# Performance work log

Hardware: AMD Instinct MI355X
Metric: run time of the kernel (lower is better)

The kernel has to match this reference:

```python
import jax, jax.numpy as jnp
import numpy as np

EPS = 1e-5  # BatchNorm1d default eps


def gcn_conv(x, src, dst, w, b, n):
    # src/dst already include self-loops. Symmetric normalization D^-1/2 (A+I) D^-1/2.
    deg = jnp.zeros((n,), x.dtype).at[dst].add(1.0)
    dinv = jnp.where(deg > 0, jax.lax.rsqrt(jnp.maximum(deg, 1.0)), 0.0)
    norm = dinv[src] * dinv[dst]                      # [E+N]
    h = x @ w                                          # [B, N, H]
    msg = h[:, src, :] * norm[None, :, None]           # gather + scale  [B, E+N, H]
    agg = jnp.zeros_like(h).at[:, dst, :].add(msg)     # scatter-add
    return agg + b


def batch_norm(h, gamma, beta):
    # training-mode BN over the flattened (B*N) axis, biased variance (torch BN forward)
    mu = h.mean(axis=(0, 1))
    var = ((h - mu) ** 2).mean(axis=(0, 1))
    return (h - mu) * jax.lax.rsqrt(var + EPS) * gamma + beta


def reference(x, edge_index, W1, b1, W2, b2, gamma1, beta1, gamma2, beta2, Wc, bc):
    n = x.shape[1]
    loops = jnp.arange(n)
    src = jnp.concatenate([edge_index[0], loops])
    dst = jnp.concatenate([edge_index[1], loops])
    h = jax.nn.relu(gcn_conv(x, src, dst, W1, b1, n))
    h = batch_norm(h, gamma1, beta1)
    # dropout(p=0.2) treated as identity (eval / deterministic reference)
    h = jax.nn.relu(gcn_conv(h, src, dst, W2, b2, n))
    h = batch_norm(h, gamma2, beta2)
    out = (h @ Wc + bc).squeeze(-1)                    # [B, N]
    return out


def setup_inputs() -> dict:
    key = jax.random.key(0)
    ks = jax.random.split(key, 8)
    B, N, E, F, H = 4, 20000, 320000, 64, 128
    s = lambda fan: 1.0 / np.sqrt(fan)
    return {
        "x": jax.random.normal(ks[0], (B, N, F), dtype=jnp.float32),
        "edge_index": jax.random.randint(ks[1], (2, E), 0, N, dtype=jnp.int64),
        "W1": jax.random.normal(ks[2], (F, H), dtype=jnp.float32) * s(F),
        "b1": jnp.zeros((H,), jnp.float32),
        "W2": jax.random.normal(ks[3], (H, H), dtype=jnp.float32) * s(H),
        "b2": jnp.zeros((H,), jnp.float32),
        "gamma1": jnp.ones((H,), jnp.float32),
        "beta1": jnp.zeros((H,), jnp.float32),
        "gamma2": jnp.ones((H,), jnp.float32),
        "beta2": jnp.zeros((H,), jnp.float32),
        "Wc": jax.random.normal(ks[4], (H, 1), dtype=jnp.float32) * s(H),
        "bc": jnp.zeros((1,), jnp.float32),
    }
```

## Files before the change

kernel.cpp:

```cpp
#include <hip/hip_runtime.h>

constexpr int Bb = 4;
constexpr int Nn = 20000;
constexpr int Ff = 64;
constexpr int Hh = 128;
constexpr float BN_EPS = 1e-5f;
constexpr int NSLOTS = 64;
constexpr int NB = (Nn + 1023) / 1024;

typedef __attribute__((ext_vector_type(8))) short bf16x8;
typedef __attribute__((ext_vector_type(4))) float f32x4;

__device__ inline unsigned f2bf(float f) {
    unsigned u = __float_as_uint(f);
    return (u + 0x7fffu + ((u >> 16) & 1u)) >> 16;
}
__device__ inline unsigned pack2(float lo, float hi) { return f2bf(lo) | (f2bf(hi) << 16); }
__device__ inline float bf_lo(unsigned w) { return __uint_as_float(w << 16); }
__device__ inline float bf_hi(unsigned w) { return __uint_as_float(w & 0xffff0000u); }

template <int NU>
__device__ inline void ldrow(unsigned* u, const unsigned* p) {
    if constexpr (NU == 2) { const uint2 t = *(const uint2*)p; u[0] = t.x; u[1] = t.y; }
    else { const uint4 t = *(const uint4*)p; u[0] = t.x; u[1] = t.y; u[2] = t.z; u[3] = t.w; }
}
template <int NU>
__device__ inline void acc_row(float* a, const unsigned* u, float nm) {
#pragma unroll
    for (int c = 0; c < NU; ++c) {
        a[2 * c]     = fmaf(nm, bf_lo(u[c]), a[2 * c]);
        a[2 * c + 1] = fmaf(nm, bf_hi(u[c]), a[2 * c + 1]);
    }
}

__global__ __launch_bounds__(256) void k_pre(const int* __restrict__ dst, int E,
                                             int NDEG,
                                             int* __restrict__ deg,
                                             const float* __restrict__ x,
                                             unsigned* __restrict__ xb,
                                             const float* __restrict__ W1,
                                             unsigned short* __restrict__ WTf) {
    const int b = blockIdx.x;
    if (b < NDEG) {
        const int e = b * 256 + threadIdx.x;
        if (e < E) atomicAdd(&deg[dst[e]], 1);
    } else if (b < NDEG + (Bb * Nn * 32) / 256) {
        const int o = (b - NDEG) * 256 + threadIdx.x;
        const int n   = o >> 7;
        const int rem = o & 127;
        const int bb  = rem >> 5;
        const int c2  = rem & 31;
        const float2 v = *(const float2*)&x[(((size_t)bb * Nn + n) * 64) + c2 * 2];
        xb[o] = pack2(v.x, v.y);
    } else {
        const int f = (b - NDEG - (Bb * Nn * 32) / 256) * 256 + threadIdx.x;
        if (f < 128 * Ff) {
            const int j = f & 7, lane = (f >> 3) & 63, rest = f >> 9;
            const int ks = rest & 1, tt = rest >> 1;
            const int col = tt * 16 + (lane & 15);
            const int k = ks * 32 + ((lane >> 4) << 3) + j;
            WTf[f] = (unsigned short)f2bf(W1[(size_t)k * 128 + col]);
        }
    }
}

__global__ __launch_bounds__(1024) void k_scanall(const int* __restrict__ deg,
                                                  int* __restrict__ rowptr,
                                                  int* __restrict__ cursor,
                                                  float* __restrict__ dinv) {
    __shared__ int red[16];
    __shared__ int woff[16];
    __shared__ int base_s;
    const int tid = threadIdx.x, lane = tid & 63, wid = tid >> 6;
    const int b = blockIdx.x;

    int pre = 0;
    for (int i = tid; i < b * 1024; i += 1024) pre += deg[i] + 1;
#pragma unroll
    for (int d = 32; d; d >>= 1) pre += __shfl_down(pre, d);
    if (lane == 0) red[wid] = pre;
    __syncthreads();
    if (tid == 0) {
        int s = 0;
        for (int w = 0; w < 16; ++w) s += red[w];
        base_s = s;
    }

    const int i = b * 1024 + tid;
    const int cnt = (i < Nn) ? deg[i] + 1 : 0;
    int v = cnt;
#pragma unroll
    for (int d = 1; d < 64; d <<= 1) {
        const int t = __shfl_up(v, d);
        if (lane >= d) v += t;
    }
    __syncthreads();
    if (lane == 63) red[wid] = v;
    __syncthreads();
    if (wid == 0) {
        const int orig = (lane < 16) ? red[lane] : 0;
        int w = orig;
#pragma unroll
        for (int d = 1; d < 16; d <<= 1) {
            const int t = __shfl_up(w, d);
            if (lane >= d) w += t;
        }
        if (lane < 16) woff[lane] = w - orig;
    }
    __syncthreads();
    if (i < Nn) {
        const int excl = base_s + woff[wid] + (v - cnt);
        rowptr[i] = excl;
        cursor[i] = excl;
        dinv[i] = rsqrtf((float)cnt);
        if (i == Nn - 1) rowptr[Nn] = excl + cnt;
    }
}

__global__ void k_fill(const int* __restrict__ src, const int* __restrict__ dst, int E,
                       const float* __restrict__ dinv, int* __restrict__ cursor,
                       int* __restrict__ csr_src, float* __restrict__ csr_norm,
                       float* __restrict__ nsum) {
    int t = blockIdx.x * blockDim.x + threadIdx.x;
    int s, d;
    if (t < E) { s = src[t]; d = dst[t]; }
    else if (t < E + Nn) { s = d = t - E; }
    else return;
    int pos = atomicAdd(&cursor[d], 1);
    const float nm = dinv[s] * dinv[d];
    csr_src[pos]  = s;
    csr_norm[pos] = nm;
    atomicAdd(&nsum[d], nm);
}

__global__ __launch_bounds__(256) void k_stat(const unsigned* __restrict__ h,
                                              float* __restrict__ gsum,
                                              float* __restrict__ gsq) {
    __shared__ float lsum[128], lsq[128];
    const int tid = threadIdx.x;
    if (tid < 128) { lsum[tid] = 0.f; lsq[tid] = 0.f; }
    __syncthreads();
    constexpr int TOTAL = Bb * Nn * (Hh / 2);
    const int stride = gridDim.x * 256;
    float s0 = 0.f, s1 = 0.f, q0 = 0.f, q1 = 0.f;
    for (int i = blockIdx.x * 256 + tid; i < TOTAL; i += stride) {
        const unsigned w = h[i];
        const float lo = bf_lo(w), hi = bf_hi(w);
        s0 += lo; s1 += hi;
        q0 = fmaf(lo, lo, q0); q1 = fmaf(hi, hi, q1);
    }
    const int c0 = (tid & 63) * 2;
    atomicAdd(&lsum[c0], s0);     atomicAdd(&lsum[c0 + 1], s1);
    atomicAdd(&lsq[c0],  q0);     atomicAdd(&lsq[c0 + 1],  q1);
    __syncthreads();
    float* gs = gsum + (size_t)(blockIdx.x & (NSLOTS - 1)) * 128;
    float* gq = gsq  + (size_t)(blockIdx.x & (NSLOTS - 1)) * 128;
    if (tid < 128) { atomicAdd(&gs[tid], lsum[tid]); atomicAdd(&gq[tid], lsq[tid]); }
}

__global__ __launch_bounds__(128) void k_prep2(const float* __restrict__ gsum,
                                               const float* __restrict__ gsq,
                                               const float* __restrict__ gamma,
                                               const float* __restrict__ beta,
                                               const float* __restrict__ W2,
                                               unsigned short* __restrict__ WT2f,
                                               float* __restrict__ shW2) {
    __shared__ float sc_s[128], sh_s[128];
    const int c = threadIdx.x;
    float s = 0.f, q = 0.f;
    for (int j = 0; j < NSLOTS; ++j) { s += gsum[j * 128 + c]; q += gsq[j * 128 + c]; }
    const float inv = 1.0f / (float)(Bb * Nn);
    const float mu  = s * inv;
    const float var = q * inv - mu * mu;
    const float sc  = gamma[c] * rsqrtf(var + BN_EPS);
    sc_s[c] = sc;
    sh_s[c] = beta[c] - mu * sc;
    __syncthreads();
    if (blockIdx.x < 64) {
#pragma unroll
        for (int i = 0; i < 2; ++i) {
            const int f = blockIdx.x * 256 + i * 128 + c;
            const int j = f & 7, lane = (f >> 3) & 63, rest = f >> 9;
            const int ks = rest & 3, tt = rest >> 2;
            const int col = tt * 16 + (lane & 15);
            const int k = ks * 32 + ((lane >> 4) << 3) + j;
            WT2f[f] = (unsigned short)f2bf(sc_s[k] * W2[(size_t)k * 128 + col]);
        }
    } else {
        float a = 0.f;
        for (int k = 0; k < 128; ++k) a = fmaf(sh_s[k], W2[(size_t)k * 128 + c], a);
        shW2[c] = a;
    }
}

template <int K, bool L2E>
__global__ __launch_bounds__(128, 8) void k_fmm(const unsigned* __restrict__ G,
                                                const int* __restrict__ rowptr,
                                                const int* __restrict__ csr_src,
                                                const float* __restrict__ csr_norm,
                                                const unsigned short* __restrict__ WTf,
                                                const float* __restrict__ bias,
                                                const float* __restrict__ nsum,
                                                const float* __restrict__ shW2,
                                                unsigned short* __restrict__ Yout) {
    constexpr int NKS = K / 32;
    constexpr int AST = K + 8;
    constexpr int NU = K / 32;
    constexpr int UNR = (K == 128) ? 4 : 8;
    constexpr int ROWU = Bb * K / 2;
    constexpr int WSLOT = 16 * AST + (K == 64 ? 1024 : 0);
    __shared__ alignas(16) unsigned short sAall[2 * WSLOT];

    const int w = threadIdx.x >> 6;
    const int lane = threadIdx.x & 63;
    unsigned short* const sA = &sAall[w * WSLOT];
    unsigned short* const sO = (K == 64) ? &sA[16 * AST] : &sA[8 * AST];

    const int cg = lane & 15, kg = lane >> 4;
    const int g = blockIdx.x * 2 + w;
    const int row0 = g * 8;

#pragma unroll
    for (int j = 0; j < 2; ++j) {
        const int v = g * 2 + j;
        const int beg = rowptr[v], end = rowptr[v + 1];
        float a[2 * NU];
#pragma unroll
        for (int c = 0; c < 2 * NU; ++c) a[c] = 0.f;
        int e = beg;
        for (; e + UNR <= end; e += UNR) {
            unsigned u[UNR][NU];
            int si[UNR];
#pragma unroll
            for (int q = 0; q < UNR; ++q) si[q] = csr_src[e + q];
#pragma unroll
            for (int q = 0; q < UNR; ++q)
                ldrow<NU>(u[q], G + (size_t)si[q] * ROWU + lane * NU);
#pragma unroll
            for (int q = 0; q < UNR; ++q) acc_row<NU>(a, u[q], csr_norm[e + q]);
        }
        for (; e < end; ++e) {
            unsigned u[NU];
            ldrow<NU>(u, G + (size_t)csr_src[e] * ROWU + lane * NU);
            acc_row<NU>(a, u, csr_norm[e]);
        }
        const int row = j * 4 + kg;
        unsigned p[NU];
#pragma unroll
        for (int c = 0; c < NU; ++c) p[c] = pack2(a[2 * c], a[2 * c + 1]);
        if constexpr (NU == 2) *(uint2*)&sA[row * AST + cg * 4] = *(const uint2*)p;
        else                   *(uint4*)&sA[row * AST + cg * 8] = *(const uint4*)p;
    }

    f32x4 acc[8];
#pragma unroll
    for (int t = 0; t < 8; ++t) acc[t] = (f32x4){0.f, 0.f, 0.f, 0.f};
#pragma unroll
    for (int ks = 0; ks < NKS; ++ks) {
        const bf16x8 av = *(const bf16x8*)&sA[cg * AST + ks * 32 + kg * 8];
#pragma unroll
        for (int t = 0; t < 8; ++t) {
            const bf16x8 bv = *(const bf16x8*)&WTf[(size_t)((t * NKS + ks) * 64 + lane) * 8];
            acc[t] = __builtin_amdgcn_mfma_f32_16x16x32_bf16(av, bv, acc[t], 0, 0, 0);
        }
    }

    if (kg < 2) {
        const int rbase = kg * 4;
        float ns = 0.f;
        if (L2E) ns = nsum[g * 2 + kg];
#pragma unroll
        for (int t = 0; t < 8; ++t) {
            const int col = t * 16 + cg;
            float badd = bias[col];
            if (L2E) badd = fmaf(ns, shW2[col], badd);
#pragma unroll
            for (int jj = 0; jj < 4; ++jj) {
                const float y = fmaxf(acc[t][jj] + badd, 0.f);
                sO[(rbase + jj) * 128 + col] = (unsigned short)f2bf(y);
            }
        }
    }
    const size_t obase = (size_t)row0 * 128;
#pragma unroll
    for (int h = 0; h < 2; ++h) {
        const int i16 = h * 64 + lane;
        *(uint4*)&Yout[obase + (size_t)i16 * 8] = *(const uint4*)&sO[i16 * 8];
    }
}

__global__ void k_bnfin2(const float* __restrict__ gsum, const float* __restrict__ gsq,
                         const float* __restrict__ gamma, const float* __restrict__ beta,
                         const float* __restrict__ Wc, const float* __restrict__ bc,
                         float* __restrict__ wcs, float* __restrict__ kc) {
    __shared__ float red[128];
    const int c = threadIdx.x;
    float s = 0.f, q = 0.f;
    for (int j = 0; j < NSLOTS; ++j) { s += gsum[j * 128 + c]; q += gsq[j * 128 + c]; }
    const float inv = 1.0f / (float)(Bb * Nn);
    const float mu  = s * inv;
    const float var = q * inv - mu * mu;
    const float sc  = gamma[c] * rsqrtf(var + BN_EPS);
    const float sh  = beta[c] - mu * sc;
    const float w   = Wc[c];
    wcs[c] = sc * w;
    red[c] = sh * w;
    __syncthreads();
    for (int st = 64; st; st >>= 1) {
        if (c < st) red[c] += red[c + st];
        __syncthreads();
    }
    if (c == 0) kc[0] = red[0] + bc[0];
}

__global__ __launch_bounds__(256) void k_cls(const unsigned* __restrict__ h2,
                                             const float* __restrict__ wcs,
                                             const float* __restrict__ kc,
                                             float* __restrict__ out) {
    __shared__ float sres[64];
    const int w = threadIdx.x >> 6;
    const int lane = threadIdx.x & 63;
    const int n0 = blockIdx.x * 16;
    const float2 wc = *(const float2*)&wcs[lane * 2];
#pragma unroll
    for (int jj = 0; jj < 4; ++jj) {
        const int node = n0 + w * 4 + jj;
#pragma unroll
        for (int b = 0; b < 4; ++b) {
            const size_t row = (size_t)node * 4 + b;
            const unsigned hv = h2[row * 64 + lane];
            float p = bf_lo(hv) * wc.x + bf_hi(hv) * wc.y;
#pragma unroll
            for (int off = 32; off; off >>= 1) p += __shfl_down(p, off);
            if (lane == 0) sres[b * 16 + w * 4 + jj] = p;
        }
    }
    __syncthreads();
    if (threadIdx.x < 64) {
        const int b = threadIdx.x >> 4, i = threadIdx.x & 15;
        out[(size_t)b * Nn + n0 + i] = sres[b * 16 + i] + kc[0];
    }
}

extern "C" void kernel_launch(void* const* d_in, const int* in_sizes, int n_in,
                              void* d_out, int out_size, void* d_ws, size_t ws_size,
                              hipStream_t stream) {
    const float* x      = (const float*)d_in[0];
    const int*   ei     = (const int*)d_in[1];
    const float* W1     = (const float*)d_in[2];
    const float* b1     = (const float*)d_in[3];
    const float* W2     = (const float*)d_in[4];
    const float* b2     = (const float*)d_in[5];
    const float* gamma1 = (const float*)d_in[6];
    const float* beta1  = (const float*)d_in[7];
    const float* gamma2 = (const float*)d_in[8];
    const float* beta2  = (const float*)d_in[9];
    const float* Wc     = (const float*)d_in[10];
    const float* bc     = (const float*)d_in[11];
    float* out = (float*)d_out;

    const int E = in_sizes[1] / 2;
    const int* src = ei;
    const int* dst = ei + E;

    char* ws = (char*)d_ws;
    size_t off = 0;
    auto alloc = [&](size_t bytes) -> char* {
        char* p = ws + off;
        off += (bytes + 255) & ~(size_t)255;
        return p;
    };
    int*      deg      = (int*)     alloc((size_t)Nn * 4);
    float*    nsum     = (float*)   alloc((size_t)Nn * 4);
    float*    gstat    = (float*)   alloc((size_t)4 * NSLOTS * 128 * 4);
    const size_t zspan = (size_t)((char*)(gstat + 4 * NSLOTS * 128) - (char*)deg);
    float* gsum1 = gstat;
    float* gsq1  = gstat + NSLOTS * 128;
    float* gsum2 = gstat + 2 * NSLOTS * 128;
    float* gsq2  = gstat + 3 * NSLOTS * 128;

    int*      cursor   = (int*)     alloc((size_t)Nn * 4);
    int*      rowptr   = (int*)     alloc((size_t)(Nn + 1) * 4);
    float*    dinv     = (float*)   alloc((size_t)Nn * 4);
    int*      csr_src  = (int*)     alloc((size_t)(E + Nn) * 4);
    float*    csr_norm = (float*)   alloc((size_t)(E + Nn) * 4);
    float*    wcs      = (float*)   alloc(128 * 4);
    float*    kc       = (float*)   alloc(256);
    unsigned short* WT1f = (unsigned short*)alloc((size_t)128 * Ff * 2);
    unsigned short* WT2f = (unsigned short*)alloc((size_t)128 * Hh * 2);
    float*          shW2 = (float*)         alloc((size_t)128 * 4);
    unsigned*       xb   = (unsigned*)      alloc((size_t)Nn * Bb * 32 * 4);
    unsigned short* h1b  = (unsigned short*)alloc((size_t)Bb * Nn * Hh * 2);
    unsigned short* h2b  = (unsigned short*)alloc((size_t)Bb * Nn * Hh * 2);

    (void)hipMemsetAsync(deg, 0, zspan, stream);

    const int NDEG = (E + 255) / 256;
    const int NCVT = (Bb * Nn * 32) / 256;
    k_pre<<<NDEG + NCVT + 32, 256, 0, stream>>>(dst, E, NDEG, deg, x, xb, W1, WT1f);
    k_scanall<<<NB, 1024, 0, stream>>>(deg, rowptr, cursor, dinv);
    k_fill<<<(E + Nn + 255) / 256, 256, 0, stream>>>(src, dst, E, dinv, cursor,
                                                     csr_src, csr_norm, nsum);

    k_fmm<Ff, false><<<Nn / 4, 128, 0, stream>>>(
        xb, rowptr, csr_src, csr_norm, WT1f, b1, nullptr, nullptr, h1b);
    k_stat<<<640, 256, 0, stream>>>((const unsigned*)h1b, gsum1, gsq1);
    k_prep2<<<65, 128, 0, stream>>>(gsum1, gsq1, gamma1, beta1, W2, WT2f, shW2);
    k_fmm<Hh, true><<<Nn / 4, 128, 0, stream>>>(
        (const unsigned*)h1b, rowptr, csr_src, csr_norm, WT2f, b2, nsum, shW2, h2b);
    k_stat<<<640, 256, 0, stream>>>((const unsigned*)h2b, gsum2, gsq2);
    k_bnfin2<<<1, Hh, 0, stream>>>(gsum2, gsq2, gamma2, beta2, Wc, bc, wcs, kc);

    k_cls<<<Nn / 16, 256, 0, stream>>>((const unsigned*)h2b, wcs, kc, out);
}
```

Measured before the change: 218.4 us.

## Fuse BatchNorm statistics into GCN aggregation-matmul epilogue, one wave per block

```diff
diff --git a/kernel.cpp b/kernel.cpp
--- a/kernel.cpp
+++ b/kernel.cpp
@@ -133,31 +133,6 @@
     atomicAdd(&nsum[d], nm);
 }
 
-__global__ __launch_bounds__(256) void k_stat(const unsigned* __restrict__ h,
-                                              float* __restrict__ gsum,
-                                              float* __restrict__ gsq) {
-    __shared__ float lsum[128], lsq[128];
-    const int tid = threadIdx.x;
-    if (tid < 128) { lsum[tid] = 0.f; lsq[tid] = 0.f; }
-    __syncthreads();
-    constexpr int TOTAL = Bb * Nn * (Hh / 2);
-    const int stride = gridDim.x * 256;
-    float s0 = 0.f, s1 = 0.f, q0 = 0.f, q1 = 0.f;
-    for (int i = blockIdx.x * 256 + tid; i < TOTAL; i += stride) {
-        const unsigned w = h[i];
-        const float lo = bf_lo(w), hi = bf_hi(w);
-        s0 += lo; s1 += hi;
-        q0 = fmaf(lo, lo, q0); q1 = fmaf(hi, hi, q1);
-    }
-    const int c0 = (tid & 63) * 2;
-    atomicAdd(&lsum[c0], s0);     atomicAdd(&lsum[c0 + 1], s1);
-    atomicAdd(&lsq[c0],  q0);     atomicAdd(&lsq[c0 + 1],  q1);
-    __syncthreads();
-    float* gs = gsum + (size_t)(blockIdx.x & (NSLOTS - 1)) * 128;
-    float* gq = gsq  + (size_t)(blockIdx.x & (NSLOTS - 1)) * 128;
-    if (tid < 128) { atomicAdd(&gs[tid], lsum[tid]); atomicAdd(&gq[tid], lsq[tid]); }
-}
-
 __global__ __launch_bounds__(128) void k_prep2(const float* __restrict__ gsum,
                                                const float* __restrict__ gsq,
                                                const float* __restrict__ gamma,
@@ -194,50 +169,57 @@
 }
 
 template <int K, bool L2E>
-__global__ __launch_bounds__(128, 8) void k_fmm(const unsigned* __restrict__ G,
-                                                const int* __restrict__ rowptr,
-                                                const int* __restrict__ csr_src,
-                                                const float* __restrict__ csr_norm,
-                                                const unsigned short* __restrict__ WTf,
-                                                const float* __restrict__ bias,
-                                                const float* __restrict__ nsum,
-                                                const float* __restrict__ shW2,
-                                                unsigned short* __restrict__ Yout) {
+__global__ __launch_bounds__(64, 6) void k_fmm(const unsigned* __restrict__ G,
+                                               const int* __restrict__ rowptr,
+                                               const int* __restrict__ csr_src,
+                                               const float* __restrict__ csr_norm,
+                                               const unsigned short* __restrict__ WTf,
+                                               const float* __restrict__ bias,
+                                               const float* __restrict__ nsum,
+                                               const float* __restrict__ shW2,
+                                               unsigned short* __restrict__ Yout,
+                                               float* __restrict__ gsum,
+                                               float* __restrict__ gsq) {
     constexpr int NKS = K / 32;
     constexpr int AST = K + 8;
     constexpr int NU = K / 32;
-    constexpr int UNR = (K == 128) ? 4 : 8;
     constexpr int ROWU = Bb * K / 2;
-    constexpr int WSLOT = 16 * AST + (K == 64 ? 1024 : 0);
-    __shared__ alignas(16) unsigned short sAall[2 * WSLOT];
-
-    const int w = threadIdx.x >> 6;
-    const int lane = threadIdx.x & 63;
-    unsigned short* const sA = &sAall[w * WSLOT];
-    unsigned short* const sO = (K == 64) ? &sA[16 * AST] : &sA[8 * AST];
-
+    __shared__ alignas(16) unsigned short sA[16 * AST];
+
+    const int lane = threadIdx.x;
     const int cg = lane & 15, kg = lane >> 4;
-    const int g = blockIdx.x * 2 + w;
-    const int row0 = g * 8;
-
-#pragma unroll
-    for (int j = 0; j < 2; ++j) {
-        const int v = g * 2 + j;
+    const int g = blockIdx.x;
+    const int row0 = g * 16;
+
+#pragma unroll
+    for (int j = 0; j < 4; ++j) {
+        const int v = g * 4 + j;
         const int beg = rowptr[v], end = rowptr[v + 1];
         float a[2 * NU];
 #pragma unroll
         for (int c = 0; c < 2 * NU; ++c) a[c] = 0.f;
         int e = beg;
-        for (; e + UNR <= end; e += UNR) {
-            unsigned u[UNR][NU];
-            int si[UNR];
-#pragma unroll
-            for (int q = 0; q < UNR; ++q) si[q] = csr_src[e + q];
-#pragma unroll
-            for (int q = 0; q < UNR; ++q)
+        for (; e + 8 <= end; e += 8) {
+            unsigned u[8][NU];
+            int si[8];
+#pragma unroll
+            for (int q = 0; q < 8; ++q) si[q] = csr_src[e + q];
+#pragma unroll
+            for (int q = 0; q < 8; ++q)
                 ldrow<NU>(u[q], G + (size_t)si[q] * ROWU + lane * NU);
 #pragma unroll
-            for (int q = 0; q < UNR; ++q) acc_row<NU>(a, u[q], csr_norm[e + q]);
+            for (int q = 0; q < 8; ++q) acc_row<NU>(a, u[q], csr_norm[e + q]);
+        }
+        for (; e + 4 <= end; e += 4) {
+            unsigned u[4][NU];
+            int si[4];
+#pragma unroll
+            for (int q = 0; q < 4; ++q) si[q] = csr_src[e + q];
+#pragma unroll
+            for (int q = 0; q < 4; ++q)
+                ldrow<NU>(u[q], G + (size_t)si[q] * ROWU + lane * NU);
+#pragma unroll
+            for (int q = 0; q < 4; ++q) acc_row<NU>(a, u[q], csr_norm[e + q]);
         }
         for (; e < end; ++e) {
             unsigned u[NU];
@@ -265,27 +247,26 @@
         }
     }
 
-    if (kg < 2) {
-        const int rbase = kg * 4;
-        float ns = 0.f;
-        if (L2E) ns = nsum[g * 2 + kg];
-#pragma unroll
-        for (int t = 0; t < 8; ++t) {
-            const int col = t * 16 + cg;
-            float badd = bias[col];
-            if (L2E) badd = fmaf(ns, shW2[col], badd);
-#pragma unroll
-            for (int jj = 0; jj < 4; ++jj) {
-                const float y = fmaxf(acc[t][jj] + badd, 0.f);
-                sO[(rbase + jj) * 128 + col] = (unsigned short)f2bf(y);
-            }
-        }
-    }
-    const size_t obase = (size_t)row0 * 128;
-#pragma unroll
-    for (int h = 0; h < 2; ++h) {
-        const int i16 = h * 64 + lane;
-        *(uint4*)&Yout[obase + (size_t)i16 * 8] = *(const uint4*)&sO[i16 * 8];
+    const int rbase = kg * 4;
+    float ns = 0.f;
+    if (L2E) ns = nsum[g * 4 + kg];
+    float* gs = gsum + (size_t)(g & (NSLOTS - 1)) * 128;
+    float* gq = gsq  + (size_t)(g & (NSLOTS - 1)) * 128;
+#pragma unroll
+    for (int t = 0; t < 8; ++t) {
+        const int col = t * 16 + cg;
+        float badd = bias[col];
+        if (L2E) badd = fmaf(ns, shW2[col], badd);
+        float s = 0.f, q = 0.f;
+#pragma unroll
+        for (int jj = 0; jj < 4; ++jj) {
+            const float y = fmaxf(acc[t][jj] + badd, 0.f);
+            Yout[(size_t)(row0 + rbase + jj) * 128 + col] = (unsigned short)f2bf(y);
+            s += y; q = fmaf(y, y, q);
+        }
+        s += __shfl_xor(s, 16); s += __shfl_xor(s, 32);
+        q += __shfl_xor(q, 16); q += __shfl_xor(q, 32);
+        if (kg == 0) { atomicAdd(&gs[col], s); atomicAdd(&gq[col], q); }
     }
 }
 
@@ -402,13 +383,12 @@
     k_fill<<<(E + Nn + 255) / 256, 256, 0, stream>>>(src, dst, E, dinv, cursor,
                                                      csr_src, csr_norm, nsum);
 
-    k_fmm<Ff, false><<<Nn / 4, 128, 0, stream>>>(
-        xb, rowptr, csr_src, csr_norm, WT1f, b1, nullptr, nullptr, h1b);
-    k_stat<<<640, 256, 0, stream>>>((const unsigned*)h1b, gsum1, gsq1);
+    k_fmm<Ff, false><<<Nn / 4, 64, 0, stream>>>(
+        xb, rowptr, csr_src, csr_norm, WT1f, b1, nullptr, nullptr, h1b, gsum1, gsq1);
     k_prep2<<<65, 128, 0, stream>>>(gsum1, gsq1, gamma1, beta1, W2, WT2f, shW2);
-    k_fmm<Hh, true><<<Nn / 4, 128, 0, stream>>>(
-        (const unsigned*)h1b, rowptr, csr_src, csr_norm, WT2f, b2, nsum, shW2, h2b);
-    k_stat<<<640, 256, 0, stream>>>((const unsigned*)h2b, gsum2, gsq2);
+    k_fmm<Hh, true><<<Nn / 4, 64, 0, stream>>>(
+        (const unsigned*)h1b, rowptr, csr_src, csr_norm, WT2f, b2, nsum, shW2,
+        h2b, gsum2, gsq2);
     k_bnfin2<<<1, Hh, 0, stream>>>(gsum2, gsq2, gamma2, beta2, Wc, bc, wcs, kc);
 
     k_cls<<<Nn / 16, 256, 0, stream>>>((const unsigned*)h2b, wcs, kc, out);
```

New measurement: 178.7 us. 1.22x faster.
